# Kernel tuning notes

Measured on AMD Instinct MI355X. Metric: run time of the kernel, lower is better.

Reference implementation:

```python
import jax, jax.numpy as jnp
import numpy as np
from jax import lax

VOCAB, EMB, RNN = 20000, 300, 512
B, NCLS, TWORDS = 64, 200, 8


def setup_inputs() -> dict:
    key = jax.random.key(0)
    ks = jax.random.split(key, 10)
    s = 0.05
    return {
        "sentence": jax.random.randint(ks[0], (B, NCLS, TWORDS), 0, VOCAB, dtype=jnp.int32),
        "word2vec": jax.random.normal(ks[1], (VOCAB, EMB), dtype=jnp.float32) * s,
        "W_ih1": jax.random.normal(ks[2], (4 * RNN, EMB), dtype=jnp.float32) * s,
        "W_hh1": jax.random.normal(ks[3], (4 * RNN, RNN), dtype=jnp.float32) * s,
        "b_ih1": jax.random.normal(ks[4], (4 * RNN,), dtype=jnp.float32) * s,
        "b_hh1": jax.random.normal(ks[5], (4 * RNN,), dtype=jnp.float32) * s,
        "W_ih2": jax.random.normal(ks[6], (4 * RNN, RNN), dtype=jnp.float32) * s,
        "W_hh2": jax.random.normal(ks[7], (4 * RNN, RNN), dtype=jnp.float32) * s,
        "b_ih2": jax.random.normal(ks[8], (4 * RNN,), dtype=jnp.float32) * s,
        "b_hh2": jax.random.normal(ks[9], (4 * RNN,), dtype=jnp.float32) * s,
    }


def _lstm_cell(x, h, c, W_ih, W_hh, b):
    # PyTorch LSTMCell gate order: i, f, g, o
    gates = x @ W_ih.T + h @ W_hh.T + b  # [BN, 4*RNN]
    i, f, g, o = jnp.split(gates, 4, axis=-1)
    c_new = jax.nn.sigmoid(f) * c + jax.nn.sigmoid(i) * jnp.tanh(g)
    h_new = jax.nn.sigmoid(o) * jnp.tanh(c_new)
    return h_new, c_new


def reference(sentence, word2vec, W_ih1, W_hh1, b_ih1, b_hh1, W_ih2, W_hh2, b_ih2, b_hh2):
    batch, num_class, max_words = sentence.shape
    bn = batch * num_class
    ids = sentence.reshape(bn, max_words)
    # embedding gather + tanh (dropout is identity in eval mode)
    emb = jnp.tanh(word2vec[ids])              # [BN, T, EMB]
    xs = jnp.swapaxes(emb, 0, 1)               # [T, BN, EMB]
    b1 = b_ih1 + b_hh1
    b2 = b_ih2 + b_hh2
    rnn = W_hh1.shape[1]
    zeros = jnp.zeros((bn, rnn), dtype=word2vec.dtype)
    init = (zeros, zeros, zeros, zeros)

    def step(carry, x):
        h1, c1, h2, c2 = carry
        h1, c1 = _lstm_cell(x, h1, c1, W_ih1, W_hh1, b1)
        h2, c2 = _lstm_cell(h1, h2, c2, W_ih2, W_hh2, b2)
        return (h1, c1, h2, c2), None

    (h1, c1, h2, c2), _ = lax.scan(step, init, xs)
    return h2.reshape(batch, num_class, rnn)
```

## Files before the change

kernel.cpp:

```cpp
#include <hip/hip_runtime.h>
#include <hip/hip_bf16.h>

#define BROWS  12800
#define TSTEPS 8
#define EMB    300
#define EMBP   320
#define RNN    512
#define NG     2048
#define K1     832
#define K2     1024

typedef short bf16x8 __attribute__((ext_vector_type(8)));
typedef float f32x4  __attribute__((ext_vector_type(4)));
typedef __hip_bfloat16 bf16;

__device__ __forceinline__ float sigmoidf_(float x) { return 1.f / (1.f + __expf(-x)); }
__device__ __forceinline__ float tanhf_(float x)    { return 1.f - 2.f / (__expf(2.f * x) + 1.f); }

__device__ __forceinline__ void gl_lds16(const bf16* g, bf16* l) {
    __builtin_amdgcn_global_load_lds(
        (const __attribute__((address_space(1))) void*)g,
        (__attribute__((address_space(3))) void*)l,
        16, 0, 0);
}

__global__ void convert_weights(const float* __restrict__ Wih1, const float* __restrict__ Whh1,
                                const float* __restrict__ Wih2, const float* __restrict__ Whh2,
                                const float* __restrict__ bih1, const float* __restrict__ bhh1,
                                const float* __restrict__ bih2, const float* __restrict__ bhh2,
                                bf16* __restrict__ Wc1, bf16* __restrict__ Wc2,
                                float* __restrict__ Bp1, float* __restrict__ Bp2) {
    int idx = blockIdx.x * 256 + threadIdx.x;
    const int n1 = NG * K1;
    const int n2 = NG * K2;
    if (idx < n1) {
        int n = idx / K1, k = idx - n * K1;
        int on = ((n >> 4) & 3) * RNN + (n >> 6) * 16 + (n & 15);
        float v = 0.f;
        if (k < EMB)        v = Wih1[on * EMB + k];
        else if (k >= EMBP) v = Whh1[on * RNN + (k - EMBP)];
        Wc1[idx] = __float2bfloat16(v);
    }
    if (idx < n2) {
        int n = idx >> 10, k = idx & (K2 - 1);
        int on = ((n >> 4) & 3) * RNN + (n >> 6) * 16 + (n & 15);
        float v = (k < RNN) ? Wih2[on * RNN + k] : Whh2[on * RNN + (k - RNN)];
        Wc2[idx] = __float2bfloat16(v);
    }
    if (idx < NG) {
        int on = ((idx >> 4) & 3) * RNN + (idx >> 6) * 16 + (idx & 15);
        Bp1[idx] = bih1[on] + bhh1[on];
        Bp2[idx] = bih2[on] + bhh2[on];
    }
}

__global__ void embed_step(const int* __restrict__ sent, const float* __restrict__ w2v,
                           bf16* __restrict__ Xbuf, int t) {
    int row = blockIdx.x;
    int col = threadIdx.x;
    int id  = sent[row * TSTEPS + t];
    float v = (col < EMB) ? tanhf_(w2v[id * EMB + col]) : 0.f;
    Xbuf[(size_t)row * EMBP + col] = __float2bfloat16(v);
}

#define BM 128
#define BN 128

__global__ __launch_bounds__(256, 4) void gemm_lstm(const bf16* __restrict__ Ax, int ldx, int ksplit,
                                                    const bf16* __restrict__ Ah, int ldh_in,
                                                    const bf16* __restrict__ W, int ldw,
                                                    const float* __restrict__ Bp,
                                                    float* __restrict__ cst,
                                                    bf16* __restrict__ hdst, int ldh_out, int offh,
                                                    float* __restrict__ outf, int en_out,
                                                    int Kl) {
    __shared__ __attribute__((aligned(16))) bf16 sA[BM * 64];
    __shared__ __attribute__((aligned(16))) bf16 sB[BN * 64];

    const int tid  = threadIdx.x;
    const int lane = tid & 63;
    const int wave = tid >> 6;
    const int wm   = wave >> 1, wn = wave & 1;
    const int bn   = blockIdx.x;
    const int bm   = blockIdx.y;

    f32x4 acc[4][4];
#pragma unroll
    for (int i = 0; i < 4; ++i)
#pragma unroll
        for (int j = 0; j < 4; ++j)
#pragma unroll
            for (int r = 0; r < 4; ++r) acc[i][j][r] = 0.f;

    const int r = lane & 15, q = lane >> 4;

    int srow[4], scol[4];
#pragma unroll
    for (int c = 0; c < 4; ++c) {
        int ch = c * 256 + tid;
        srow[c] = ch >> 3;
        scol[c] = ((ch & 7) ^ (srow[c] & 7)) * 8;
    }
    const bf16* Wbase = W + (size_t)(bn * BN) * ldw;

    for (int kb = 0; kb < Kl; kb += 64) {
        const bf16* src; int ld, ko;
        if (kb < ksplit) { src = Ax; ld = ldx;    ko = kb; }
        else             { src = Ah; ld = ldh_in; ko = kb - ksplit; }
        src += (size_t)(bm * BM) * ld;
#pragma unroll
        for (int c = 0; c < 4; ++c) {
            int ch = c * 256 + tid;
            gl_lds16(src   + (size_t)srow[c] * ld  + ko + scol[c], &sA[ch * 8]);
            gl_lds16(Wbase + (size_t)srow[c] * ldw + kb + scol[c], &sB[ch * 8]);
        }
        __syncthreads();
#pragma unroll
        for (int kk = 0; kk < 64; kk += 32) {
            const int kc = kk >> 3;
            bf16x8 af[4], wf[4];
#pragma unroll
            for (int i = 0; i < 4; ++i)
                af[i] = *(const bf16x8*)(&sA[(wm * 64 + i * 16 + r) * 64 + (((q + kc) ^ (r & 7)) * 8)]);
#pragma unroll
            for (int j = 0; j < 4; ++j)
                wf[j] = *(const bf16x8*)(&sB[(wn * 64 + j * 16 + r) * 64 + (((q + kc) ^ (r & 7)) * 8)]);
#pragma unroll
            for (int i = 0; i < 4; ++i)
#pragma unroll
                for (int j = 0; j < 4; ++j)
                    acc[i][j] = __builtin_amdgcn_mfma_f32_16x16x32_bf16(
                        af[i], wf[j], acc[i][j], 0, 0, 0);
        }
        __syncthreads();
    }

    const int colb = bn * BN + wn * 64;
    const int u    = (2 * bn + wn) * 16 + r;
    const float bi = Bp[colb + r];
    const float bf = Bp[colb + 16 + r];
    const float bg = Bp[colb + 32 + r];
    const float bo = Bp[colb + 48 + r];

    float cc[4][4];
#pragma unroll
    for (int i = 0; i < 4; ++i)
#pragma unroll
        for (int rr = 0; rr < 4; ++rr) {
            int row = bm * BM + wm * 64 + i * 16 + q * 4 + rr;
            cc[i][rr] = cst[(size_t)row * RNN + u];
        }

#define HLD 40
#pragma unroll
    for (int i = 0; i < 4; ++i) {
#pragma unroll
        for (int rr = 0; rr < 4; ++rr) {
            int rowl = wm * 64 + i * 16 + q * 4 + rr;
            int row  = bm * BM + rowl;
            size_t cidx = (size_t)row * RNN + u;
            float gi = acc[i][0][rr] + bi;
            float gf = acc[i][1][rr] + bf;
            float gg = acc[i][2][rr] + bg;
            float go = acc[i][3][rr] + bo;
            float cn = sigmoidf_(gf) * cc[i][rr] + sigmoidf_(gi) * tanhf_(gg);
            float h  = sigmoidf_(go) * tanhf_(cn);
            cst[cidx] = cn;
            if (en_out) outf[cidx] = h;
            sA[rowl * HLD + wn * 16 + r] = __float2bfloat16(h);
        }
    }
    __syncthreads();

#pragma unroll
    for (int half = 0; half < 2; ++half) {
        int t    = half * 256 + tid;
        int rowl = t >> 2;
        int c8   = (t & 3) * 8;
        uint4 v  = *(const uint4*)&sA[rowl * HLD + c8];
        int row  = bm * BM + rowl;
        int gcol = bn * 32 + c8;
        *(uint4*)&hdst[(size_t)row * ldh_out + offh + gcol] = v;
    }
#undef HLD
}

extern "C" void kernel_launch(void* const* d_in, const int* in_sizes, int n_in,
                              void* d_out, int out_size, void* d_ws, size_t ws_size,
                              hipStream_t stream) {
    (void)in_sizes; (void)n_in; (void)out_size; (void)ws_size;
    const int*   sent = (const int*)d_in[0];
    const float* w2v  = (const float*)d_in[1];
    const float* Wih1 = (const float*)d_in[2];
    const float* Whh1 = (const float*)d_in[3];
    const float* bih1 = (const float*)d_in[4];
    const float* bhh1 = (const float*)d_in[5];
    const float* Wih2 = (const float*)d_in[6];
    const float* Whh2 = (const float*)d_in[7];
    const float* bih2 = (const float*)d_in[8];
    const float* bhh2 = (const float*)d_in[9];
    float* out = (float*)d_out;

    char* ws = (char*)d_ws;
    float* c1   = (float*)(ws);
    float* c2   = (float*)(ws + 26214400);
    bf16*  A2[2];
    A2[0] = (bf16*)(ws + 52428800);
    A2[1] = (bf16*)(ws + 78643200);
    bf16*  Xbuf = (bf16*) (ws + 104857600);
    bf16*  Wc1  = (bf16*) (ws + 113049600);
    bf16*  Wc2  = (bf16*) (ws + 116457472);
    float* Bp1  = (float*)(ws + 120651776);
    float* Bp2  = (float*)(ws + 120659968);

    hipMemsetAsync(ws, 0, 52428800, stream);

    convert_weights<<<dim3((NG * K2 + 255) / 256), dim3(256), 0, stream>>>(
        Wih1, Whh1, Wih2, Whh2, bih1, bhh1, bih2, bhh2, Wc1, Wc2, Bp1, Bp2);

    for (int t = 0; t < TSTEPS; ++t) {
        const int cur = t & 1, prv = cur ^ 1;

        embed_step<<<dim3(BROWS), dim3(EMBP), 0, stream>>>(sent, w2v, Xbuf, t);

        gemm_lstm<<<dim3(NG / BN, BROWS / BM), dim3(256), 0, stream>>>(
            Xbuf, EMBP, EMBP,
            A2[prv], K2,
            Wc1, K1, Bp1, c1,
            A2[cur], K2, 0,
            (float*)nullptr, 0,
            (t == 0) ? EMBP : K1);

        gemm_lstm<<<dim3(NG / BN, BROWS / BM), dim3(256), 0, stream>>>(
            (const bf16*)nullptr, 0, 0,
            A2[cur], K2,
            Wc2, K2, Bp2, c2,
            A2[prv], K2, RNN,
            out, (t == TSTEPS - 1) ? 1 : 0,
            (t == 0) ? RNN : K2);
    }
}
```

Baseline: 1.146 ms.

## Wavefront-fuse layer-1 and layer-2 LSTM steps and gather pre-tanh'd embeddings in GEMM

Precomputes tanh of the whole embedding table once in bf16, then has the layer-1 GEMM gather embedding rows directly by token id instead of running a per-step embed kernel. Layer 1 at step s and layer 2 at step s-1 run in one launch using a grid z-dimension role split, since they only depend on the previous step's buffer. This cuts the launch count from 24 to 10 and raises per-launch parallelism. In exchange it adds a tanh pass over the full vocabulary table and a double-buffered layout that is harder to get right.

```diff
diff --git a/kernel.cpp b/kernel.cpp
--- a/kernel.cpp
+++ b/kernel.cpp
@@ -9,6 +9,7 @@
 #define NG     2048
 #define K1     832
 #define K2     1024
+#define VOCAB  20000
 
 typedef short bf16x8 __attribute__((ext_vector_type(8)));
 typedef float f32x4  __attribute__((ext_vector_type(4)));
@@ -54,26 +55,26 @@
     }
 }
 
-__global__ void embed_step(const int* __restrict__ sent, const float* __restrict__ w2v,
-                           bf16* __restrict__ Xbuf, int t) {
+__global__ void tanh_w2v(const float* __restrict__ w2v, bf16* __restrict__ W2Vt) {
     int row = blockIdx.x;
     int col = threadIdx.x;
-    int id  = sent[row * TSTEPS + t];
-    float v = (col < EMB) ? tanhf_(w2v[id * EMB + col]) : 0.f;
-    Xbuf[(size_t)row * EMBP + col] = __float2bfloat16(v);
+    float v = (col < EMB) ? tanhf_(w2v[row * EMB + col]) : 0.f;
+    W2Vt[(size_t)row * EMBP + col] = __float2bfloat16(v);
 }
 
 #define BM 128
 #define BN 128
 
-__global__ __launch_bounds__(256, 4) void gemm_lstm(const bf16* __restrict__ Ax, int ldx, int ksplit,
-                                                    const bf16* __restrict__ Ah, int ldh_in,
-                                                    const bf16* __restrict__ W, int ldw,
-                                                    const float* __restrict__ Bp,
-                                                    float* __restrict__ cst,
-                                                    bf16* __restrict__ hdst, int ldh_out, int offh,
-                                                    float* __restrict__ outf, int en_out,
-                                                    int Kl) {
+__global__ __launch_bounds__(256, 4) void gemm_lstm(
+        int role_base, int t,
+        const bf16* __restrict__ W2Vt, const int* __restrict__ sent,
+        const bf16* __restrict__ Asrc,
+        bf16* __restrict__ hdst,
+        const bf16* __restrict__ Wc1, const bf16* __restrict__ Wc2,
+        const float* __restrict__ Bp1, const float* __restrict__ Bp2,
+        float* __restrict__ cst1, float* __restrict__ cst2,
+        float* __restrict__ outf, int en_out,
+        int Kl1, int Kl2) {
     __shared__ __attribute__((aligned(16))) bf16 sA[BM * 64];
     __shared__ __attribute__((aligned(16))) bf16 sB[BN * 64];
 
@@ -83,6 +84,12 @@
     const int wm   = wave >> 1, wn = wave & 1;
     const int bn   = blockIdx.x;
     const int bm   = blockIdx.y;
+    const int role = blockIdx.z + role_base;
+
+    const bf16*  W;  int ldw, Kl, ksplit, offh;
+    const float* Bp; float* cst;
+    if (role) { W = Wc1; ldw = K1; Kl = Kl1; ksplit = EMBP; offh = 0;   Bp = Bp1; cst = cst1; }
+    else      { W = Wc2; ldw = K2; Kl = Kl2; ksplit = 0;    offh = RNN; Bp = Bp2; cst = cst2; }
 
     f32x4 acc[4][4];
 #pragma unroll
@@ -101,17 +108,26 @@
         srow[c] = ch >> 3;
         scol[c] = ((ch & 7) ^ (srow[c] & 7)) * 8;
     }
+
+    int idv[4];
+    if (role) {
+#pragma unroll
+        for (int c = 0; c < 4; ++c)
+            idv[c] = sent[(size_t)(bm * BM + srow[c]) * TSTEPS + t];
+    }
+
     const bf16* Wbase = W + (size_t)(bn * BN) * ldw;
+    const bf16* Abase = Asrc + (size_t)(bm * BM) * K2;
 
     for (int kb = 0; kb < Kl; kb += 64) {
-        const bf16* src; int ld, ko;
-        if (kb < ksplit) { src = Ax; ld = ldx;    ko = kb; }
-        else             { src = Ah; ld = ldh_in; ko = kb - ksplit; }
-        src += (size_t)(bm * BM) * ld;
+        const bool xreg = (kb < ksplit);
 #pragma unroll
         for (int c = 0; c < 4; ++c) {
             int ch = c * 256 + tid;
-            gl_lds16(src   + (size_t)srow[c] * ld  + ko + scol[c], &sA[ch * 8]);
+            const bf16* alane = xreg
+                ? W2Vt  + (size_t)idv[c] * EMBP + kb + scol[c]
+                : Abase + (size_t)srow[c] * K2 + (kb - ksplit) + scol[c];
+            gl_lds16(alane, &sA[ch * 8]);
             gl_lds16(Wbase + (size_t)srow[c] * ldw + kb + scol[c], &sB[ch * 8]);
         }
         __syncthreads();
@@ -174,13 +190,13 @@
 
 #pragma unroll
     for (int half = 0; half < 2; ++half) {
-        int t    = half * 256 + tid;
-        int rowl = t >> 2;
-        int c8   = (t & 3) * 8;
+        int t2   = half * 256 + tid;
+        int rowl = t2 >> 2;
+        int c8   = (t2 & 3) * 8;
         uint4 v  = *(const uint4*)&sA[rowl * HLD + c8];
         int row  = bm * BM + rowl;
         int gcol = bn * 32 + c8;
-        *(uint4*)&hdst[(size_t)row * ldh_out + offh + gcol] = v;
+        *(uint4*)&hdst[(size_t)row * K2 + offh + gcol] = v;
     }
 #undef HLD
 }
@@ -207,36 +223,39 @@
     bf16*  A2[2];
     A2[0] = (bf16*)(ws + 52428800);
     A2[1] = (bf16*)(ws + 78643200);
-    bf16*  Xbuf = (bf16*) (ws + 104857600);
-    bf16*  Wc1  = (bf16*) (ws + 113049600);
-    bf16*  Wc2  = (bf16*) (ws + 116457472);
-    float* Bp1  = (float*)(ws + 120651776);
-    float* Bp2  = (float*)(ws + 120659968);
+    bf16*  W2Vt = (bf16*) (ws + 104857600);
+    bf16*  Wc1  = (bf16*) (ws + 117657600);
+    bf16*  Wc2  = (bf16*) (ws + 121065472);
+    float* Bp1  = (float*)(ws + 125259776);
+    float* Bp2  = (float*)(ws + 125267968);
 
     hipMemsetAsync(ws, 0, 52428800, stream);
 
     convert_weights<<<dim3((NG * K2 + 255) / 256), dim3(256), 0, stream>>>(
         Wih1, Whh1, Wih2, Whh2, bih1, bhh1, bih2, bhh2, Wc1, Wc2, Bp1, Bp2);
 
-    for (int t = 0; t < TSTEPS; ++t) {
-        const int cur = t & 1, prv = cur ^ 1;
-
-        embed_step<<<dim3(BROWS), dim3(EMBP), 0, stream>>>(sent, w2v, Xbuf, t);
-
-        gemm_lstm<<<dim3(NG / BN, BROWS / BM), dim3(256), 0, stream>>>(
-            Xbuf, EMBP, EMBP,
-            A2[prv], K2,
-            Wc1, K1, Bp1, c1,
-            A2[cur], K2, 0,
+    tanh_w2v<<<dim3(VOCAB), dim3(EMBP), 0, stream>>>(w2v, W2Vt);
+
+    gemm_lstm<<<dim3(NG / BN, BROWS / BM, 1), dim3(256), 0, stream>>>(
+        1, 0, W2Vt, sent,
+        A2[1] , A2[0],
+        Wc1, Wc2, Bp1, Bp2, c1, c2,
+        (float*)nullptr, 0,
+        EMBP , 0 );
+
+    for (int s = 1; s <= 7; ++s) {
+        gemm_lstm<<<dim3(NG / BN, BROWS / BM, 2), dim3(256), 0, stream>>>(
+            0, s, W2Vt, sent,
+            A2[(s - 1) & 1], A2[s & 1],
+            Wc1, Wc2, Bp1, Bp2, c1, c2,
             (float*)nullptr, 0,
-            (t == 0) ? EMBP : K1);
-
-        gemm_lstm<<<dim3(NG / BN, BROWS / BM), dim3(256), 0, stream>>>(
-            (const bf16*)nullptr, 0, 0,
-            A2[cur], K2,
-            Wc2, K2, Bp2, c2,
-            A2[prv], K2, RNN,
-            out, (t == TSTEPS - 1) ? 1 : 0,
-            (t == 0) ? RNN : K2);
-    }
-}
+            K1 , (s == 1) ? RNN : K2 );
+    }
+
+    gemm_lstm<<<dim3(NG / BN, BROWS / BM, 1), dim3(256), 0, stream>>>(
+        0, 0 , W2Vt, sent,
+        A2[1], A2[0],
+        Wc1, Wc2, Bp1, Bp2, c1, c2,
+        out, 1,
+        K1 , K2 );
+}
```

Result: faster. 1.037 ms (-9.5%).
